# Optimization experiments

Hardware: AMD Instinct MI355X
Metric: run time of the kernel (lower is better)

Reference implementation:

```python
import jax, jax.numpy as jnp
import numpy as np

H = 50  # hidden_size
IN = 1  # input_size

def _lstm_layer(x_tbi, w_ih, w_hh, b):
    # x_tbi: [T, B, in]; w_ih: [4H, in]; w_hh: [4H, H]; b: [4H] (b_ih + b_hh combined)
    T, B, _ = x_tbi.shape
    def step(carry, x_t):
        h, c = carry
        z = x_t @ w_ih.T + h @ w_hh.T + b  # [B, 4H]
        i, f, g, o = jnp.split(z, 4, axis=-1)
        i = jax.nn.sigmoid(i); f = jax.nn.sigmoid(f)
        g = jnp.tanh(g); o = jax.nn.sigmoid(o)
        c = f * c + i * g
        h = o * jnp.tanh(c)
        return (h, c), h
    h0 = jnp.zeros((B, H), x_tbi.dtype)
    c0 = jnp.zeros((B, H), x_tbi.dtype)
    _, hs = jax.lax.scan(step, (h0, c0), x_tbi)
    return hs  # [T, B, H]

def setup_inputs() -> dict:
    key = jax.random.key(0)
    ks = jax.random.split(key, 12)
    def u(k, shape, fan):
        s = 1.0 / np.sqrt(fan)
        return jax.random.uniform(k, shape, jnp.float32, -s, s)
    B, T = 2048, 512
    x = jax.random.normal(ks[0], (B, T, IN), jnp.float32)
    return {
        'x': x,
        'w_ih1': u(ks[1], (4 * H, IN), H), 'w_hh1': u(ks[2], (4 * H, H), H), 'b1': u(ks[3], (4 * H,), H),
        'w_ih2': u(ks[4], (4 * H, H), H), 'w_hh2': u(ks[5], (4 * H, H), H), 'b2': u(ks[6], (4 * H,), H),
        'w_ih3': u(ks[7], (4 * H, H), H), 'w_hh3': u(ks[8], (4 * H, H), H), 'b3': u(ks[9], (4 * H,), H),
        'w_fc': u(ks[10], (1, H), H), 'b_fc': u(ks[11], (1,), H),
    }

def reference(x, w_ih1, w_hh1, b1, w_ih2, w_hh2, b2, w_ih3, w_hh3, b3, w_fc, b_fc):
    # dropout layers act as identity in eval mode
    out = jnp.transpose(x, (1, 0, 2))  # [T, B, in]
    out = _lstm_layer(out, w_ih1, w_hh1, b1)
    out = _lstm_layer(out, w_ih2, w_hh2, b2)
    out = _lstm_layer(out, w_ih3, w_hh3, b3)
    last = out[-1]  # [B, H]
    return last @ w_fc.T + b_fc  # [B, 1]
```

## Files before the change

### kernel.cpp

```cpp
#include <hip/hip_runtime.h>
#include <math.h>

namespace {

constexpr int Hn = 50;
constexpr int Bn = 2048;
constexpr int Tn = 512;
constexpr int SW = 72;

constexpr float KS1f = -1.44269504088896340736f;
constexpr float KS2f = -2.88539008177792681472f;

typedef short short8 __attribute__((ext_vector_type(8)));
typedef float f32x4 __attribute__((ext_vector_type(4)));

__device__ __forceinline__ unsigned bcu(float f) { return __builtin_bit_cast(unsigned, f); }
__device__ __forceinline__ float bcf(unsigned u) { return __builtin_bit_cast(float, u); }
__device__ __forceinline__ float rcpa(float x) { return __builtin_amdgcn_rcpf(x); }

__device__ __forceinline__ float fexp2(float x) {
#if defined(__has_builtin)
#if __has_builtin(__builtin_amdgcn_exp2f)
  return __builtin_amdgcn_exp2f(x);
#else
  return exp2f(x);
#endif
#else
  return exp2f(x);
#endif
}

__device__ __forceinline__ void wsplit(short* ph, short* pl, float v) {
  const unsigned u = bcu(v);
  *ph = (short)(u >> 16);
  *pl = (short)(bcu(v - bcf(u & 0xFFFF0000u)) >> 16);
}

#define MF(a, b, c) __builtin_amdgcn_mfma_f32_16x16x32_bf16(a, b, c, 0, 0, 0)


#define LW(FI)                                                               \
  short8 FH##FI = {0, 0, 0, 0, 0, 0, 0, 0};                                  \
  short8 FL##FI = {0, 0, 0, 0, 0, 0, 0, 0};                                  \
  {                                                                          \
    const int tile_ =                                                        \
        ((FI) >= 16) ? ((L == 0 || wl != 0) ? 13 : 12)                       \
        : ((FI) >= 8) ? ((L == 0) ? 13 : (wl + 8))                           \
        : (L == 0)    ? (wl + 4 * ((FI) >> 1))                               \
                      : (wl + 4 * ((FI) >> 2));                              \
    const int chunk_ = ((FI) >= 8) ? ((FI)&3)                                \
                       : (L == 0)  ? ((FI)&1)                                \
                                   : ((FI)&3);                               \
    const int cb_ = 4 * tile_ + (nl >> 2);                                   \
    if (tile_ < 13 && cb_ < Hn) {                                            \
      const int row_ = (nl & 3) * Hn + cb_;                                  \
      const float sc_ = ((nl & 3) == 2) ? KS2f : KS1f;                       \
      _Pragma("unroll") for (int jj = 0; jj < 8; ++jj) {                     \
        const int k_ = 32 * chunk_ + quad * 8 + jj;                          \
        float wv = 0.f;                                                      \
        if (L == 0) {                                                        \
          if (k_ == 0) wv = wihL[row_];                                      \
          else if (k_ <= Hn) wv = whhL[row_ * Hn + k_ - 1];                  \
          else if (k_ == 51) wv = biasL[row_];                               \
        } else if (L == 1) {                                                 \
          if (k_ >= 1 && k_ <= Hn) wv = wihL[row_ * Hn + k_ - 1];            \
          else if (k_ == 51) wv = biasL[row_];                               \
          else if (k_ >= 64 && k_ < 64 + Hn) wv = whhL[row_ * Hn + k_ - 64]; \
        } else {                                                             \
          if (k_ < Hn) wv = wihL[row_ * Hn + k_];                            \
          else if (k_ == Hn) wv = biasL[row_];                               \
          else if (k_ >= 64 && k_ < 64 + Hn) wv = whhL[row_ * Hn + k_ - 64]; \
        }                                                                    \
        wv *= sc_;                                                           \
        const unsigned uu = bcu(wv);                                         \
        FH##FI[jj] = (short)(uu >> 16);                                      \
        FL##FI[jj] = (short)(bcu(wv - bcf(uu & 0xFFFF0000u)) >> 16);         \
      }                                                                      \
    }                                                                        \
  }

#define BINIT(J)                                                             \
  const int tile##J = wl + 4 * (J);                                          \
  const int tv##J = tile##J < 13;                                            \
  const int cell##J = 4 * tile##J + quad;                                    \
  float cs##J = 0.f, hl##J = 0.f;

#define MTM(J, FI)                                                           \
  if (tv##J) {                                                               \
    ac##J = MF(FH##FI, uh_, ac##J);                                          \
    ac##J = MF(FL##FI, uh_, ac##J);                                          \
    ac##J = MF(FH##FI, ul_, ac##J);                                          \
  }

#define MTMS2(CI)                                                            \
  {                                                                          \
    const short8 fh_ = s_f4j2[wz2][wl][CI][0][lane];                         \
    const short8 fl_ = s_f4j2[wz2][wl][CI][1][lane];                         \
    ac2 = MF(fh_, uh_, ac2);                                                 \
    ac2 = MF(fl_, uh_, ac2);                                                 \
    ac2 = MF(fh_, ul_, ac2);                                                 \
  }

#define MTMS3(CI)                                                            \
  if (tv3) {                                                                 \
    const short8 fh_ = s_f4j3[wz2][CI][0][lane];                             \
    const short8 fl_ = s_f4j3[wz2][CI][1][lane];                             \
    ac3 = MF(fh_, uh_, ac3);                                                 \
    ac3 = MF(fl_, uh_, ac3);                                                 \
    ac3 = MF(fh_, ul_, ac3);                                                 \
  }

#define MCH_L1(LC, F0, F1, F2, F3)                                           \
  {                                                                          \
    const short8 uh_ = *(const short8*)&p1h[rb][nl][32 * (LC) + quad * 8];   \
    const short8 ul_ = *(const short8*)&p1l[rb][nl][32 * (LC) + quad * 8];   \
    MTM(0, F0) MTM(1, F1) MTM(2, F2) MTM(3, F3)                              \
  }

#define MCH_L23(PH, PL, LC, CI, F0, F1)                                      \
  {                                                                          \
    const short8 uh_ = *(const short8*)&PH[rb][nl][32 * (LC) + quad * 8];    \
    const short8 ul_ = *(const short8*)&PL[rb][nl][32 * (LC) + quad * 8];    \
    MTM(0, F0) MTM(1, F1) MTMS2(CI) MTMS3(CI)                                \
  }

#define CUP(J, PH, PL, KO)                                                   \
  if (tv##J) {                                                               \
    const float I_ = rcpa(1.0f + fexp2(ac##J[0]));                           \
    const float F_ = rcpa(1.0f + fexp2(ac##J[1]));                           \
    const float G_ = fmaf(2.0f, rcpa(1.0f + fexp2(ac##J[2])), -1.0f);        \
    const float O_ = rcpa(1.0f + fexp2(ac##J[3]));                           \
    cs##J = fmaf(F_, cs##J, I_ * G_);                                        \
    const float tc_ = fmaf(2.0f, rcpa(1.0f + fexp2(cs##J * KS2f)), -1.0f);   \
    const float hv = O_ * tc_;                                               \
    hl##J = hv;                                                              \
    if (cell##J < Hn)                                                        \
      wsplit(&PH[wb][nl][(KO) + cell##J], &PL[wb][nl][(KO) + cell##J], hv);  \
  }

__global__ __launch_bounds__(768, 3) void lstm_fused(
    const float* __restrict__ xg,
    const float* __restrict__ wih1, const float* __restrict__ whh1,
    const float* __restrict__ b1, const float* __restrict__ wih2,
    const float* __restrict__ whh2, const float* __restrict__ b2,
    const float* __restrict__ wih3, const float* __restrict__ whh3,
    const float* __restrict__ b3, const float* __restrict__ wfc,
    const float* __restrict__ bfc, float* __restrict__ out)
{
  __shared__ __align__(16) short p1h[2][16][SW];
  __shared__ __align__(16) short p1l[2][16][SW];
  __shared__ __align__(16) short p2h[2][16][SW];
  __shared__ __align__(16) short p2l[2][16][SW];
  __shared__ __align__(16) short p3h[2][16][SW];
  __shared__ __align__(16) short p3l[2][16][SW];
  __shared__ __align__(16) short8 s_f4j2[2][4][4][2][64];
  __shared__ __align__(16) short8 s_f4j3[2][4][2][64];
  __shared__ float s_fc[4][16];

  const int tid = threadIdx.x;
  const int w = tid >> 6;
  const int lane = tid & 63;
  const int quad = lane >> 4;
  const int nl = lane & 15;
  const int L = (w < 4) ? 0 : (w < 8) ? 1 : 2;
  const int wl = w & 3;
  const int wz2 = (L == 2) ? 1 : 0;
  const int eb = blockIdx.x * 16;

  const float* wihL = (L == 0) ? wih1 : (L == 1) ? wih2 : wih3;
  const float* whhL = (L == 0) ? whh1 : (L == 1) ? whh2 : whh3;
  const float* biasL = (L == 0) ? b1 : (L == 1) ? b2 : b3;

  LW(0) LW(1) LW(2) LW(3) LW(4) LW(5) LW(6) LW(7)
  LW(8) LW(9) LW(10) LW(11)
  LW(16) LW(17) LW(18) LW(19)

  if (L > 0) {
    s_f4j2[wz2][wl][0][0][lane] = FH8;  s_f4j2[wz2][wl][0][1][lane] = FL8;
    s_f4j2[wz2][wl][1][0][lane] = FH9;  s_f4j2[wz2][wl][1][1][lane] = FL9;
    s_f4j2[wz2][wl][2][0][lane] = FH10; s_f4j2[wz2][wl][2][1][lane] = FL10;
    s_f4j2[wz2][wl][3][0][lane] = FH11; s_f4j2[wz2][wl][3][1][lane] = FL11;
    if (wl == 0) {
      s_f4j3[wz2][0][0][lane] = FH16; s_f4j3[wz2][0][1][lane] = FL16;
      s_f4j3[wz2][1][0][lane] = FH17; s_f4j3[wz2][1][1][lane] = FL17;
      s_f4j3[wz2][2][0][lane] = FH18; s_f4j3[wz2][2][1][lane] = FL18;
      s_f4j3[wz2][3][0][lane] = FH19; s_f4j3[wz2][3][1][lane] = FL19;
    }
  }

  BINIT(0) BINIT(1) BINIT(2) BINIT(3)

  for (int i = tid; i < 2 * 16 * SW; i += 768) {
    (&p1h[0][0][0])[i] = 0;
    (&p1l[0][0][0])[i] = 0;
    (&p2h[0][0][0])[i] = 0;
    (&p2l[0][0][0])[i] = 0;
    (&p3h[0][0][0])[i] = 0;
    (&p3l[0][0][0])[i] = 0;
  }
  __syncthreads();
  if (w == 0 && lane < 16) {
    const float xv = xg[(size_t)(eb + lane) * Tn + 0];
    wsplit(&p1h[0][lane][0], &p1l[0][lane][0], xv);
  }
  if (tid < 32) {
    const int bb = tid >> 4, bn = tid & 15;
    p1h[bb][bn][51] = (short)0x3F80;
    p2h[bb][bn][50] = (short)0x3F80;
  }
  __syncthreads();

#pragma unroll 1
  for (int i = 0; i < Tn + 2; ++i) {
    const int rb = i & 1, wb = rb ^ 1;
    if (L == 0) {
      if (i < Tn) {
        float xv = 0.f;
        if (w == 0 && lane < 16 && i + 1 < Tn)
          xv = xg[(size_t)(eb + lane) * Tn + (i + 1)];
        f32x4 ac0 = {0.f, 0.f, 0.f, 0.f};
        f32x4 ac1 = {0.f, 0.f, 0.f, 0.f};
        f32x4 ac2 = {0.f, 0.f, 0.f, 0.f};
        f32x4 ac3 = {0.f, 0.f, 0.f, 0.f};
        __builtin_amdgcn_s_setprio(1);
        MCH_L1(0, 0, 2, 4, 6)
        MCH_L1(1, 1, 3, 5, 7)
        __builtin_amdgcn_s_setprio(0);
        CUP(0, p1h, p1l, 1)
        CUP(1, p1h, p1l, 1)
        CUP(2, p1h, p1l, 1)
        CUP(3, p1h, p1l, 1)
        if (w == 0 && lane < 16)
          wsplit(&p1h[wb][lane][0], &p1l[wb][lane][0], xv);
      }
    } else if (L == 1) {
      if (i >= 1 && i <= Tn) {
        f32x4 ac0 = {0.f, 0.f, 0.f, 0.f};
        f32x4 ac1 = {0.f, 0.f, 0.f, 0.f};
        f32x4 ac2 = {0.f, 0.f, 0.f, 0.f};
        f32x4 ac3 = {0.f, 0.f, 0.f, 0.f};
        __builtin_amdgcn_s_setprio(1);
        MCH_L23(p1h, p1l, 0, 0, 0, 4)
        MCH_L23(p1h, p1l, 1, 1, 1, 5)
        MCH_L23(p2h, p2l, 0, 2, 2, 6)
        MCH_L23(p2h, p2l, 1, 3, 3, 7)
        __builtin_amdgcn_s_setprio(0);
        CUP(0, p2h, p2l, 0)
        CUP(1, p2h, p2l, 0)
        CUP(2, p2h, p2l, 0)
        CUP(3, p2h, p2l, 0)
      }
    } else {
      if (i >= 2) {
        f32x4 ac0 = {0.f, 0.f, 0.f, 0.f};
        f32x4 ac1 = {0.f, 0.f, 0.f, 0.f};
        f32x4 ac2 = {0.f, 0.f, 0.f, 0.f};
        f32x4 ac3 = {0.f, 0.f, 0.f, 0.f};
        __builtin_amdgcn_s_setprio(1);
        MCH_L23(p2h, p2l, 0, 0, 0, 4)
        MCH_L23(p2h, p2l, 1, 1, 1, 5)
        MCH_L23(p3h, p3l, 0, 2, 2, 6)
        MCH_L23(p3h, p3l, 1, 3, 3, 7)
        __builtin_amdgcn_s_setprio(0);
        CUP(0, p3h, p3l, 0)
        CUP(1, p3h, p3l, 0)
        CUP(2, p3h, p3l, 0)
        CUP(3, p3h, p3l, 0)
      }
    }
    __syncthreads();
  }

  if (L == 2) {
    float pfc = 0.f;
    if (tv0 && cell0 < Hn) pfc += hl0 * wfc[cell0];
    if (tv1 && cell1 < Hn) pfc += hl1 * wfc[cell1];
    if (tv2 && cell2 < Hn) pfc += hl2 * wfc[cell2];
    if (tv3 && cell3 < Hn) pfc += hl3 * wfc[cell3];
    pfc += __shfl_xor(pfc, 16);
    pfc += __shfl_xor(pfc, 32);
    if (lane < 16) s_fc[wl][lane] = pfc;
  }
  __syncthreads();
  if (tid < 16)
    out[eb + tid] = bfc[0] + s_fc[0][tid] + s_fc[1][tid] + s_fc[2][tid] +
                    s_fc[3][tid];
}

}

extern "C" void kernel_launch(void* const* d_in, const int* in_sizes, int n_in,
                              void* d_out, int out_size, void* d_ws, size_t ws_size,
                              hipStream_t stream) {
  const float* x    = (const float*)d_in[0];
  const float* wih1 = (const float*)d_in[1];
  const float* whh1 = (const float*)d_in[2];
  const float* b1   = (const float*)d_in[3];
  const float* wih2 = (const float*)d_in[4];
  const float* whh2 = (const float*)d_in[5];
  const float* b2   = (const float*)d_in[6];
  const float* wih3 = (const float*)d_in[7];
  const float* whh3 = (const float*)d_in[8];
  const float* b3   = (const float*)d_in[9];
  const float* wfc  = (const float*)d_in[10];
  const float* bfc  = (const float*)d_in[11];
  float* out = (float*)d_out;

  lstm_fused<<<dim3(Bn / 16), dim3(768), 0, stream>>>(
      x, wih1, whh1, b1, wih2, whh2, b2, wih3, whh3, b3, wfc, bfc, out);
}
```

Measured before the change: 911.9 us.

## Move layer 2/3 tail cell tile onto idle layer-1 waves

The fourth cell tile (cells 48-49) of layers 2 and 3 was computed by wave 0 of those layers, making it the critical path with four MFMA chains. That work now runs on layer-1 waves 1 and 2, which have fewer active tiles, so each step's load is spread more evenly across waves. The final FC reduction gains a fifth partial-sum slot for the moved cells. The risk is lengthening the layer-1 waves' step and adding LDS reads of weights and hidden states from shared memory.

```diff
diff --git a/kernel.cpp b/kernel.cpp
--- a/kernel.cpp
+++ b/kernel.cpp
@@ -101,15 +101,6 @@
     ac2 = MF(fh_, ul_, ac2);                                                 \
   }
 
-#define MTMS3(CI)                                                            \
-  if (tv3) {                                                                 \
-    const short8 fh_ = s_f4j3[wz2][CI][0][lane];                             \
-    const short8 fl_ = s_f4j3[wz2][CI][1][lane];                             \
-    ac3 = MF(fh_, uh_, ac3);                                                 \
-    ac3 = MF(fl_, uh_, ac3);                                                 \
-    ac3 = MF(fh_, ul_, ac3);                                                 \
-  }
-
 #define MCH_L1(LC, F0, F1, F2, F3)                                           \
   {                                                                          \
     const short8 uh_ = *(const short8*)&p1h[rb][nl][32 * (LC) + quad * 8];   \
@@ -121,7 +112,18 @@
   {                                                                          \
     const short8 uh_ = *(const short8*)&PH[rb][nl][32 * (LC) + quad * 8];    \
     const short8 ul_ = *(const short8*)&PL[rb][nl][32 * (LC) + quad * 8];    \
-    MTM(0, F0) MTM(1, F1) MTMS2(CI) MTMS3(CI)                                \
+    MTM(0, F0) MTM(1, F1) MTMS2(CI)                                          \
+  }
+
+#define AUX_MCH(AZ, PH, PL, LC, CI)                                          \
+  {                                                                          \
+    const short8 uh_ = *(const short8*)&PH[rb][nl][32 * (LC) + quad * 8];    \
+    const short8 ul_ = *(const short8*)&PL[rb][nl][32 * (LC) + quad * 8];    \
+    const short8 fh_ = s_f4j3[AZ][CI][0][lane];                              \
+    const short8 fl_ = s_f4j3[AZ][CI][1][lane];                              \
+    acA = MF(fh_, uh_, acA);                                                 \
+    acA = MF(fl_, uh_, acA);                                                 \
+    acA = MF(fh_, ul_, acA);                                                 \
   }
 
 #define CUP(J, PH, PL, KO)                                                   \
@@ -136,6 +138,20 @@
     hl##J = hv;                                                              \
     if (cell##J < Hn)                                                        \
       wsplit(&PH[wb][nl][(KO) + cell##J], &PL[wb][nl][(KO) + cell##J], hv);  \
+  }
+
+#define AUX_CUP(PH, PL)                                                      \
+  {                                                                          \
+    const float I_ = rcpa(1.0f + fexp2(acA[0]));                             \
+    const float F_ = rcpa(1.0f + fexp2(acA[1]));                             \
+    const float G_ = fmaf(2.0f, rcpa(1.0f + fexp2(acA[2])), -1.0f);          \
+    const float O_ = rcpa(1.0f + fexp2(acA[3]));                             \
+    csA = fmaf(F_, csA, I_ * G_);                                            \
+    const float tc_ = fmaf(2.0f, rcpa(1.0f + fexp2(csA * KS2f)), -1.0f);     \
+    const float hv = O_ * tc_;                                               \
+    hlA = hv;                                                                \
+    if (cellA < Hn)                                                          \
+      wsplit(&PH[wb][nl][cellA], &PL[wb][nl][cellA], hv);                    \
   }
 
 __global__ __launch_bounds__(768, 3) void lstm_fused(
@@ -155,7 +171,7 @@
   __shared__ __align__(16) short p3l[2][16][SW];
   __shared__ __align__(16) short8 s_f4j2[2][4][4][2][64];
   __shared__ __align__(16) short8 s_f4j3[2][4][2][64];
-  __shared__ float s_fc[4][16];
+  __shared__ float s_fc[5][16];
 
   const int tid = threadIdx.x;
   const int w = tid >> 6;
@@ -166,6 +182,7 @@
   const int wl = w & 3;
   const int wz2 = (L == 2) ? 1 : 0;
   const int eb = blockIdx.x * 16;
+  const int cellA = 48 + quad;
 
   const float* wihL = (L == 0) ? wih1 : (L == 1) ? wih2 : wih3;
   const float* whhL = (L == 0) ? whh1 : (L == 1) ? whh2 : whh3;
@@ -189,6 +206,7 @@
   }
 
   BINIT(0) BINIT(1) BINIT(2) BINIT(3)
+  float csA = 0.f, hlA = 0.f;
 
   for (int i = tid; i < 2 * 16 * SW; i += 768) {
     (&p1h[0][0][0])[i] = 0;
@@ -233,12 +251,31 @@
         if (w == 0 && lane < 16)
           wsplit(&p1h[wb][lane][0], &p1l[wb][lane][0], xv);
       }
+      if (wl == 1 && i >= 1 && i <= Tn) {
+        f32x4 acA = {0.f, 0.f, 0.f, 0.f};
+        __builtin_amdgcn_s_setprio(1);
+        AUX_MCH(0, p1h, p1l, 0, 0)
+        AUX_MCH(0, p1h, p1l, 1, 1)
+        AUX_MCH(0, p2h, p2l, 0, 2)
+        AUX_MCH(0, p2h, p2l, 1, 3)
+        __builtin_amdgcn_s_setprio(0);
+        AUX_CUP(p2h, p2l)
+      }
+      if (wl == 2 && i >= 2) {
+        f32x4 acA = {0.f, 0.f, 0.f, 0.f};
+        __builtin_amdgcn_s_setprio(1);
+        AUX_MCH(1, p2h, p2l, 0, 0)
+        AUX_MCH(1, p2h, p2l, 1, 1)
+        AUX_MCH(1, p3h, p3l, 0, 2)
+        AUX_MCH(1, p3h, p3l, 1, 3)
+        __builtin_amdgcn_s_setprio(0);
+        AUX_CUP(p3h, p3l)
+      }
     } else if (L == 1) {
       if (i >= 1 && i <= Tn) {
         f32x4 ac0 = {0.f, 0.f, 0.f, 0.f};
         f32x4 ac1 = {0.f, 0.f, 0.f, 0.f};
         f32x4 ac2 = {0.f, 0.f, 0.f, 0.f};
-        f32x4 ac3 = {0.f, 0.f, 0.f, 0.f};
         __builtin_amdgcn_s_setprio(1);
         MCH_L23(p1h, p1l, 0, 0, 0, 4)
         MCH_L23(p1h, p1l, 1, 1, 1, 5)
@@ -248,14 +285,12 @@
         CUP(0, p2h, p2l, 0)
         CUP(1, p2h, p2l, 0)
         CUP(2, p2h, p2l, 0)
-        CUP(3, p2h, p2l, 0)
       }
     } else {
       if (i >= 2) {
         f32x4 ac0 = {0.f, 0.f, 0.f, 0.f};
         f32x4 ac1 = {0.f, 0.f, 0.f, 0.f};
         f32x4 ac2 = {0.f, 0.f, 0.f, 0.f};
-        f32x4 ac3 = {0.f, 0.f, 0.f, 0.f};
         __builtin_amdgcn_s_setprio(1);
         MCH_L23(p2h, p2l, 0, 0, 0, 4)
         MCH_L23(p2h, p2l, 1, 1, 1, 5)
@@ -265,7 +300,6 @@
         CUP(0, p3h, p3l, 0)
         CUP(1, p3h, p3l, 0)
         CUP(2, p3h, p3l, 0)
-        CUP(3, p3h, p3l, 0)
       }
     }
     __syncthreads();
@@ -276,15 +310,21 @@
     if (tv0 && cell0 < Hn) pfc += hl0 * wfc[cell0];
     if (tv1 && cell1 < Hn) pfc += hl1 * wfc[cell1];
     if (tv2 && cell2 < Hn) pfc += hl2 * wfc[cell2];
-    if (tv3 && cell3 < Hn) pfc += hl3 * wfc[cell3];
     pfc += __shfl_xor(pfc, 16);
     pfc += __shfl_xor(pfc, 32);
     if (lane < 16) s_fc[wl][lane] = pfc;
   }
+  if (L == 0 && wl == 2) {
+    float pfcA = 0.f;
+    if (quad < 2) pfcA = hlA * wfc[cellA];
+    pfcA += __shfl_xor(pfcA, 16);
+    pfcA += __shfl_xor(pfcA, 32);
+    if (lane < 16) s_fc[4][lane] = pfcA;
+  }
   __syncthreads();
   if (tid < 16)
     out[eb + tid] = bfc[0] + s_fc[0][tid] + s_fc[1][tid] + s_fc[2][tid] +
-                    s_fc[3][tid];
+                    s_fc[3][tid] + s_fc[4][tid];
 }
 
 }
```

Result: faster. 767.7 us (median of 3 runs) (-15.8%).
